# Optimization experiments

Hardware: AMD Instinct MI355X
Metric: run time of the kernel (lower is better)

Reference implementation:

```python
import jax, jax.numpy as jnp
import numpy as np

FP8_E4M3_MAX = 448.0  # max finite value of float8_e4m3fn
SCALE = 2.0           # hardcoded activation scale in FP8QDQLinear.__init__
WEIGHT_SCALE = 2.0    # hardcoded weight scale


def quantize_fp8(x, scale):
    # torchao quantize_affine_float8: divide by scale, saturate to fp8 range, cast
    return jnp.clip(x / scale, -FP8_E4M3_MAX, FP8_E4M3_MAX).astype(jnp.float8_e4m3fn)


def dequantize_fp8(q, scale):
    # torchao dequantize_affine_float8: upcast to fp32 then multiply by scale
    return q.astype(jnp.float32) * scale


def setup_inputs() -> dict:
    key = jax.random.key(0)
    k1, k2, k3 = jax.random.split(key, 3)
    in_features, out_features = 4096, 4096
    inp = jax.random.normal(k1, (4, 4096, in_features), dtype=jnp.float32)
    # weight is created as randn().to(float8_e4m3fn) in __init__ (a buffer, not a Parameter)
    weight = jax.random.normal(k2, (out_features, in_features), dtype=jnp.float32).astype(jnp.float8_e4m3fn)
    bias = jax.random.normal(k3, (out_features,), dtype=jnp.float32)
    return {"input": inp, "weight": weight, "bias": bias}


def reference(input, weight, bias):
    # dequantize fp8 weight
    w = dequantize_fp8(weight, WEIGHT_SCALE)            # [O, I] fp32
    # QDQ fake-quant on activations
    dq_input = dequantize_fp8(quantize_fp8(input, SCALE), SCALE)  # [B, S, I]
    # standard linear: y = x @ W^T + b
    out = jnp.einsum('bsi,oi->bso', dq_input, w) + bias
    return out
```

## Files before the change

### kernel.cpp

```cpp
#include <hip/hip_runtime.h>

typedef float f32x4 __attribute__((ext_vector_type(4)));
typedef float f32x16 __attribute__((ext_vector_type(16)));
typedef int i32x4 __attribute__((ext_vector_type(4)));
typedef int i32x8 __attribute__((ext_vector_type(8)));

#define M_DIM 16384L
#define N_DIM 4096L
#define K_DIM 4096L

__device__ __forceinline__ unsigned int f32_to_e4m3(float x, float scale) {
  float v = fminf(fmaxf(x * scale, -448.f), 448.f);
  unsigned int u = __float_as_uint(v);
  unsigned int s = (u >> 24) & 0x80u;
  float ax = fabsf(v);
  unsigned int ua = __float_as_uint(ax);
  unsigned int subn = (unsigned int)rintf(ax * 512.0f);
  unsigned int r = ua + 0x7FFFFu + ((ua >> 20) & 1u);
  unsigned int nrm = ((r >> 20) & 0x7FFu) - 960u;
  unsigned int mag = (ax < 0.015625f) ? subn : nrm;
  return mag | s;
}

__device__ __forceinline__ unsigned int pack4_e4m3(float4 v, float scale) {
  return f32_to_e4m3(v.x, scale) | (f32_to_e4m3(v.y, scale) << 8) |
         (f32_to_e4m3(v.z, scale) << 16) | (f32_to_e4m3(v.w, scale) << 24);
}

__device__ __forceinline__ unsigned int cvt_pk4(float a, float b, float c, float d) {
  unsigned int r;
  asm("v_cvt_pk_fp8_f32 %0, %1, %2\n\t"
      "v_cvt_pk_fp8_f32 %0, %3, %4 op_sel:[0,0,1]"
      : "=&v"(r) : "v"(a), "v"(b), "v"(c), "v"(d));
  return r;
}

__device__ __forceinline__ float clampq(float x, float scale) {
  return fminf(fmaxf(x * scale, -448.f), 448.f);
}

__device__ __forceinline__ unsigned int quant4_hw(float4 v, float scale) {
  return cvt_pk4(clampq(v.x, scale), clampq(v.y, scale),
                 clampq(v.z, scale), clampq(v.w, scale));
}

__global__ __launch_bounds__(256) void quant_fp8_hw(const float* __restrict__ in,
                                                    uint4* __restrict__ out,
                                                    float scale, long n16) {
  long i = (long)blockIdx.x * 256 + threadIdx.x;
  const long stride = (long)gridDim.x * 256;
  for (; i < n16; i += stride) {
    const float4* p = reinterpret_cast<const float4*>(in) + i * 4;
    float4 v0 = p[0], v1 = p[1], v2 = p[2], v3 = p[3];
    uint4 r;
    r.x = quant4_hw(v0, scale);
    r.y = quant4_hw(v1, scale);
    r.z = quant4_hw(v2, scale);
    r.w = quant4_hw(v3, scale);
    out[i] = r;
  }
}

__device__ __forceinline__ void gld_lds16(const unsigned char* g, unsigned char* l) {
  __builtin_amdgcn_global_load_lds(
      (const __attribute__((address_space(1))) unsigned int*)g,
      (__attribute__((address_space(3))) unsigned int*)l,
      16, 0, 0);
}

__device__ __forceinline__ uint4 quant16(const float* p, float scale) {
  const float4* q = reinterpret_cast<const float4*>(p);
  uint4 r;
  r.x = pack4_e4m3(q[0], scale);
  r.y = pack4_e4m3(q[1], scale);
  r.z = pack4_e4m3(q[2], scale);
  r.w = pack4_e4m3(q[3], scale);
  return r;
}

#define MFMA_SC(a, b, c) \
  __builtin_amdgcn_mfma_scale_f32_32x32x64_f8f6f4((a), (b), (c), 0, 0, 0, 0x7F7F7F7F, 0, 0x7F7F7F7F)

template <bool FA, bool FB>
__global__ __launch_bounds__(256) void gemm_fp8(const unsigned char* __restrict__ A8,
                                                const float* __restrict__ Af,
                                                const unsigned char* __restrict__ B8,
                                                const float* __restrict__ Bf,
                                                const float* __restrict__ bias,
                                                float* __restrict__ C) {
  __shared__ unsigned char sA[128 * 64];
  __shared__ unsigned char sB[128 * 64];

  const int t = threadIdx.x;
  const int lane = t & 63;
  const int w = t >> 6;
  const int wm = w >> 1;
  const int wn = w & 1;
  const long bx = blockIdx.x;
  const long by = blockIdx.y;

  f32x16 acc[2][2] = {};

  const int l0 = w * 64 + lane;
  const int l1 = l0 + 256;
  const int r0 = l0 >> 2, c0 = (l0 & 3) ^ ((l0 >> 3) & 3);
  const int r1 = l1 >> 2, c1 = (l1 & 3) ^ ((l1 >> 3) & 3);

  const unsigned char* gA0 = nullptr; const unsigned char* gA1 = nullptr;
  const float* fA0 = nullptr;         const float* fA1 = nullptr;
  if constexpr (FA) {
    fA0 = Af + (by * 128 + r0) * K_DIM + c0 * 16;
    fA1 = Af + (by * 128 + r1) * K_DIM + c1 * 16;
  } else {
    gA0 = A8 + (by * 128 + r0) * K_DIM + c0 * 16;
    gA1 = A8 + (by * 128 + r1) * K_DIM + c1 * 16;
  }
  const unsigned char* gB0 = nullptr; const unsigned char* gB1 = nullptr;
  const float* fB0 = nullptr;         const float* fB1 = nullptr;
  if constexpr (FB) {
    fB0 = Bf + (bx * 128 + r0) * K_DIM + c0 * 16;
    fB1 = Bf + (bx * 128 + r1) * K_DIM + c1 * 16;
  } else {
    gB0 = B8 + (bx * 128 + r0) * K_DIM + c0 * 16;
    gB1 = B8 + (bx * 128 + r1) * K_DIM + c1 * 16;
  }

  unsigned char* lA0 = sA + w * 1024;
  unsigned char* lA1 = sA + 4096 + w * 1024;
  unsigned char* lB0 = sB + w * 1024;
  unsigned char* lB1 = sB + 4096 + w * 1024;

  const int r32 = lane & 31;
  const int key = (lane >> 1) & 3;
  const int p_lo = ((lane >> 5) << 1) ^ key;
  const unsigned char* sAw = sA + wm * 4096;
  const unsigned char* sBw = sB + wn * 4096;

  for (int kt = 0; kt < (int)(K_DIM / 64); ++kt) {
    if constexpr (FA) {
      *reinterpret_cast<uint4*>(sA + l0 * 16) = quant16(fA0, 0.5f);
      *reinterpret_cast<uint4*>(sA + l1 * 16) = quant16(fA1, 0.5f);
      fA0 += 64; fA1 += 64;
    } else {
      gld_lds16(gA0, lA0);
      gld_lds16(gA1, lA1);
      gA0 += 64; gA1 += 64;
    }
    if constexpr (FB) {
      *reinterpret_cast<uint4*>(sB + l0 * 16) = quant16(fB0, 1.0f);
      *reinterpret_cast<uint4*>(sB + l1 * 16) = quant16(fB1, 1.0f);
      fB0 += 64; fB1 += 64;
    } else {
      gld_lds16(gB0, lB0);
      gld_lds16(gB1, lB1);
      gB0 += 64; gB1 += 64;
    }
    __syncthreads();

    i32x8 af[2], bf[2];
#pragma unroll
    for (int i = 0; i < 2; ++i) {
      const unsigned char* pa = sAw + (i * 32 + r32) * 64;
      i32x4 alo = *reinterpret_cast<const i32x4*>(pa + p_lo * 16);
      i32x4 ahi = *reinterpret_cast<const i32x4*>(pa + (p_lo ^ 1) * 16);
      af[i] = i32x8{alo[0], alo[1], alo[2], alo[3], ahi[0], ahi[1], ahi[2], ahi[3]};
      const unsigned char* pb = sBw + (i * 32 + r32) * 64;
      i32x4 blo = *reinterpret_cast<const i32x4*>(pb + p_lo * 16);
      i32x4 bhi = *reinterpret_cast<const i32x4*>(pb + (p_lo ^ 1) * 16);
      bf[i] = i32x8{blo[0], blo[1], blo[2], blo[3], bhi[0], bhi[1], bhi[2], bhi[3]};
    }

#pragma unroll
    for (int i = 0; i < 2; ++i) {
#pragma unroll
      for (int j = 0; j < 2; ++j) {
        acc[i][j] = MFMA_SC(af[i], bf[j], acc[i][j]);
      }
    }
    __syncthreads();
  }

  const int mrow = 4 * (lane >> 5);
  const long gm_base = by * 128 + wm * 64;
  const long gn_base = bx * 128 + wn * 64 + r32;
#pragma unroll
  for (int nj = 0; nj < 2; ++nj) {
    const long gn = gn_base + nj * 32;
    const float bv = bias[gn];
#pragma unroll
    for (int mi = 0; mi < 2; ++mi) {
#pragma unroll
      for (int r = 0; r < 16; ++r) {
        const long gm = gm_base + mi * 32 + (r & 3) + 8 * (r >> 2) + mrow;
        C[gm * N_DIM + gn] = acc[mi][nj][r] * 4.0f + bv;
      }
    }
  }
}

extern "C" void kernel_launch(void* const* d_in, const int* in_sizes, int n_in,
                              void* d_out, int out_size, void* d_ws, size_t ws_size,
                              hipStream_t stream) {
  const float* inp = (const float*)d_in[0];
  const float* wgt = (const float*)d_in[1];
  const float* bias = (const float*)d_in[2];
  float* out = (float*)d_out;

  dim3 grid((unsigned)(N_DIM / 128), (unsigned)(M_DIM / 128));
  const size_t A_BYTES = (size_t)(M_DIM * K_DIM);
  const size_t B_BYTES = (size_t)(N_DIM * K_DIM);

  if (ws_size >= A_BYTES + B_BYTES) {
    unsigned char* aq = (unsigned char*)d_ws;
    unsigned char* wq = (unsigned char*)d_ws + A_BYTES;
    quant_fp8_hw<<<dim3(2048), dim3(256), 0, stream>>>(
        inp, (uint4*)aq, 0.5f, M_DIM * K_DIM / 16);
    quant_fp8_hw<<<dim3(2048), dim3(256), 0, stream>>>(
        wgt, (uint4*)wq, 1.0f, N_DIM * K_DIM / 16);
    gemm_fp8<false, false><<<grid, dim3(256), 0, stream>>>(aq, nullptr, wq, nullptr, bias, out);
  } else if (ws_size >= B_BYTES) {
    unsigned char* wq = (unsigned char*)d_ws;
    quant_fp8_hw<<<dim3(2048), dim3(256), 0, stream>>>(
        wgt, (uint4*)wq, 1.0f, N_DIM * K_DIM / 16);
    gemm_fp8<true, false><<<grid, dim3(256), 0, stream>>>(nullptr, inp, wq, nullptr, bias, out);
  } else {
    gemm_fp8<true, true><<<grid, dim3(256), 0, stream>>>(nullptr, inp, nullptr, wgt, bias, out);
  }
}
```

Before: 779.6 us.

## Use two-wave GEMM blocks with 64x128 per-wave tiles and MFMA priority

Adds a GEMM variant that keeps the 128x128 block tile but splits it across two waves instead of four. Each wave computes a 64x128 output sub-tile with eight MFMAs per k-step, which raises MFMA work per LDS fragment load and reuses the B fragments across both A fragments. Each thread issues four A and four B global-to-LDS loads per step, and s_setprio raises wave priority around the MFMA burst. The costs are higher register pressure from 8 accumulators and fewer waves per block to hide latency.

```diff
diff --git a/kernel.cpp b/kernel.cpp
--- a/kernel.cpp
+++ b/kernel.cpp
@@ -78,8 +78,87 @@
   return r;
 }
 
+__device__ __forceinline__ i32x8 ldfrag(const unsigned char* p, int p_lo) {
+  i32x4 lo = *reinterpret_cast<const i32x4*>(p + p_lo * 16);
+  i32x4 hi = *reinterpret_cast<const i32x4*>(p + (p_lo ^ 1) * 16);
+  return i32x8{lo[0], lo[1], lo[2], lo[3], hi[0], hi[1], hi[2], hi[3]};
+}
+
 #define MFMA_SC(a, b, c) \
   __builtin_amdgcn_mfma_scale_f32_32x32x64_f8f6f4((a), (b), (c), 0, 0, 0, 0x7F7F7F7F, 0, 0x7F7F7F7F)
+
+__global__ __launch_bounds__(128, 2) void gemm_fp8_w2(
+    const unsigned char* __restrict__ A8, const unsigned char* __restrict__ B8,
+    const float* __restrict__ bias, float* __restrict__ C) {
+  __shared__ unsigned char sA[128 * 64];
+  __shared__ unsigned char sB[128 * 64];
+
+  const int t = threadIdx.x;
+  const int lane = t & 63;
+  const int w = t >> 6;
+  const long bx = blockIdx.x;
+  const long by = blockIdx.y;
+
+  f32x16 acc[2][4] = {};
+
+  const int srow = t >> 2;
+  const int sc = (t & 3) ^ ((t >> 3) & 3);
+  const unsigned char* gA = A8 + (by * 128 + srow) * K_DIM + sc * 16;
+  const unsigned char* gB = B8 + (bx * 128 + srow) * K_DIM + sc * 16;
+  const long rstep = 32 * K_DIM;
+  const int wofs = w * 1024;
+
+  const int r32 = lane & 31;
+  const int key = (lane >> 1) & 3;
+  const int p_lo = ((lane >> 5) << 1) ^ key;
+  const unsigned char* sAw = sA + w * 4096;
+
+  for (int kt = 0; kt < (int)(K_DIM / 64); ++kt) {
+#pragma unroll
+    for (int j = 0; j < 4; ++j) {
+      gld_lds16(gA + j * rstep, sA + wofs + j * 2048);
+      gld_lds16(gB + j * rstep, sB + wofs + j * 2048);
+    }
+    gA += 64; gB += 64;
+    __syncthreads();
+
+    i32x8 af0 = ldfrag(sAw + r32 * 64, p_lo);
+    i32x8 af1 = ldfrag(sAw + (32 + r32) * 64, p_lo);
+    i32x8 bf0 = ldfrag(sB + r32 * 64, p_lo);
+    i32x8 bf1 = ldfrag(sB + (32 + r32) * 64, p_lo);
+    i32x8 bf2 = ldfrag(sB + (64 + r32) * 64, p_lo);
+    i32x8 bf3 = ldfrag(sB + (96 + r32) * 64, p_lo);
+
+    __builtin_amdgcn_s_setprio(1);
+    acc[0][0] = MFMA_SC(af0, bf0, acc[0][0]);
+    acc[0][1] = MFMA_SC(af0, bf1, acc[0][1]);
+    acc[0][2] = MFMA_SC(af0, bf2, acc[0][2]);
+    acc[0][3] = MFMA_SC(af0, bf3, acc[0][3]);
+    acc[1][0] = MFMA_SC(af1, bf0, acc[1][0]);
+    acc[1][1] = MFMA_SC(af1, bf1, acc[1][1]);
+    acc[1][2] = MFMA_SC(af1, bf2, acc[1][2]);
+    acc[1][3] = MFMA_SC(af1, bf3, acc[1][3]);
+    __builtin_amdgcn_s_setprio(0);
+    __syncthreads();
+  }
+
+  const int mrow = 4 * (lane >> 5);
+  const long gm_base = by * 128 + w * 64;
+  const long gn_base = bx * 128 + r32;
+#pragma unroll
+  for (int nj = 0; nj < 4; ++nj) {
+    const long gn = gn_base + nj * 32;
+    const float bv = bias[gn];
+#pragma unroll
+    for (int mi = 0; mi < 2; ++mi) {
+#pragma unroll
+      for (int r = 0; r < 16; ++r) {
+        const long gm = gm_base + mi * 32 + (r & 3) + 8 * (r >> 2) + mrow;
+        C[gm * N_DIM + gn] = acc[mi][nj][r] * 4.0f + bv;
+      }
+    }
+  }
+}
 
 template <bool FA, bool FB>
 __global__ __launch_bounds__(256) void gemm_fp8(const unsigned char* __restrict__ A8,
@@ -160,14 +239,8 @@
     i32x8 af[2], bf[2];
 #pragma unroll
     for (int i = 0; i < 2; ++i) {
-      const unsigned char* pa = sAw + (i * 32 + r32) * 64;
-      i32x4 alo = *reinterpret_cast<const i32x4*>(pa + p_lo * 16);
-      i32x4 ahi = *reinterpret_cast<const i32x4*>(pa + (p_lo ^ 1) * 16);
-      af[i] = i32x8{alo[0], alo[1], alo[2], alo[3], ahi[0], ahi[1], ahi[2], ahi[3]};
-      const unsigned char* pb = sBw + (i * 32 + r32) * 64;
-      i32x4 blo = *reinterpret_cast<const i32x4*>(pb + p_lo * 16);
-      i32x4 bhi = *reinterpret_cast<const i32x4*>(pb + (p_lo ^ 1) * 16);
-      bf[i] = i32x8{blo[0], blo[1], blo[2], blo[3], bhi[0], bhi[1], bhi[2], bhi[3]};
+      af[i] = ldfrag(sAw + (i * 32 + r32) * 64, p_lo);
+      bf[i] = ldfrag(sBw + (i * 32 + r32) * 64, p_lo);
     }
 
 #pragma unroll
@@ -217,7 +290,7 @@
         inp, (uint4*)aq, 0.5f, M_DIM * K_DIM / 16);
     quant_fp8_hw<<<dim3(2048), dim3(256), 0, stream>>>(
         wgt, (uint4*)wq, 1.0f, N_DIM * K_DIM / 16);
-    gemm_fp8<false, false><<<grid, dim3(256), 0, stream>>>(aq, nullptr, wq, nullptr, bias, out);
+    gemm_fp8_w2<<<grid, dim3(128), 0, stream>>>(aq, wq, bias, out);
   } else if (ws_size >= B_BYTES) {
     unsigned char* wq = (unsigned char*)d_ws;
     quant_fp8_hw<<<dim3(2048), dim3(256), 0, stream>>>(
```

After: 781.8 us. Within noise of the previous version (+0.3%).
